# Optimization experiments

Hardware: AMD Instinct MI355X
Metric: run time of the kernel (lower is better)

The kernel has to match this reference:

```python
import jax, jax.numpy as jnp
import numpy as np

NEG_SLOPE = 0.2  # PyG GATConv leaky_relu slope


def _gat_layer(x, src, dst, W, a_src, a_dst, b, concat, num_nodes):
    # x: [N, F_in], W: [F_in, H*C], a_src/a_dst: [H, C], b: [H*C] or [C]
    H, C = a_src.shape
    h = (x @ W).reshape(num_nodes, H, C)                      # [N, H, C]
    s_src = jnp.einsum('nhc,hc->nh', h, a_src)                # [N, H]
    s_dst = jnp.einsum('nhc,hc->nh', h, a_dst)                # [N, H]
    e = jax.nn.leaky_relu(s_src[src] + s_dst[dst], NEG_SLOPE) # [E, H]
    # segment softmax over edges sharing a destination node
    m = jax.ops.segment_max(e, dst, num_segments=num_nodes)
    m = jnp.where(jnp.isfinite(m), m, 0.0)
    p = jnp.exp(e - m[dst])
    z = jax.ops.segment_sum(p, dst, num_segments=num_nodes)
    alpha = p / (z[dst] + 1e-16)                              # [E, H]
    msg = h[src] * alpha[:, :, None]                          # [E, H, C]
    out = jax.ops.segment_sum(msg, dst, num_segments=num_nodes)  # [N, H, C]
    out = out.reshape(num_nodes, H * C) if concat else out.mean(axis=1)
    return out + b


def setup_inputs() -> dict:
    key = jax.random.key(0)
    ks = jax.random.split(key, 16)
    N, E, F = 100000, 800000, 128
    H, C = 4, 32
    sc_in = 1.0 / np.sqrt(F)
    inp = {
        'x': jax.random.normal(ks[0], (N, F), jnp.float32),
        'edge_index': jax.random.randint(ks[1], (2, E), 0, N, jnp.int64),
        'W1': jax.random.normal(ks[2], (F, H * C), jnp.float32) * sc_in,
        'a_src1': jax.random.normal(ks[3], (H, C), jnp.float32),
        'a_dst1': jax.random.normal(ks[4], (H, C), jnp.float32),
        'b1': jax.random.normal(ks[5], (H * C,), jnp.float32) * 0.01,
        'W2': jax.random.normal(ks[6], (F, H * C), jnp.float32) * sc_in,
        'a_src2': jax.random.normal(ks[7], (H, C), jnp.float32),
        'a_dst2': jax.random.normal(ks[8], (H, C), jnp.float32),
        'b2': jax.random.normal(ks[9], (H * C,), jnp.float32) * 0.01,
        'W3': jax.random.normal(ks[10], (F, H * F), jnp.float32) * sc_in,
        'a_src3': jax.random.normal(ks[11], (H, F), jnp.float32),
        'a_dst3': jax.random.normal(ks[12], (H, F), jnp.float32),
        'b3': jax.random.normal(ks[13], (F,), jnp.float32) * 0.01,
    }
    return inp


def reference(x, edge_index, W1, a_src1, a_dst1, b1, W2, a_src2, a_dst2, b2,
              W3, a_src3, a_dst3, b3):
    N = x.shape[0]
    # PyG GATConv default: add self loops
    loop = jnp.arange(N, dtype=edge_index.dtype)
    src = jnp.concatenate([edge_index[0], loop])
    dst = jnp.concatenate([edge_index[1], loop])
    # conv1 (concat heads) + residual + ELU
    x1 = jax.nn.elu(_gat_layer(x, src, dst, W1, a_src1, a_dst1, b1, True, N) + x)
    # intermediate conv (concat heads) + residual + ELU
    x2 = jax.nn.elu(_gat_layer(x1, src, dst, W2, a_src2, a_dst2, b2, True, N) + x1)
    # final conv (mean over heads) + residual, no ELU
    x3 = _gat_layer(x2, src, dst, W3, a_src3, a_dst3, b3, False, N) + x2
    return x3
```

## Files before the change

kernel.cpp:

```cpp
#include <hip/hip_runtime.h>
#include <hip/hip_bf16.h>
#include <cstdint>

#define NEG_SLOPE 0.2f

typedef __bf16 bf16x8 __attribute__((ext_vector_type(8)));
typedef _Float16 half8 __attribute__((ext_vector_type(8)));
typedef float  floatx4 __attribute__((ext_vector_type(4)));

__device__ __forceinline__ float us2f(unsigned short u) {
    union { unsigned int i; float f; } c; c.i = ((unsigned int)u) << 16; return c.f;
}
__device__ __forceinline__ unsigned short f2us(float f) {
    union { float f; unsigned int i; } c; c.f = f;
    unsigned int x = c.i;
    unsigned int r = (x + 0x7fffu + ((x >> 16) & 1u)) >> 16;
    return (unsigned short)r;
}
__device__ __forceinline__ unsigned short f2h(float f) {
    union { _Float16 h; unsigned short u; } c; c.h = (_Float16)f; return c.u;
}
__device__ __forceinline__ float h2f(unsigned short u) {
    union { _Float16 h; unsigned short u; } c; c.u = u; return (float)c.h;
}
__device__ __forceinline__ float ldx(const void* p, int i, int bf) {
    return bf ? us2f(((const unsigned short*)p)[i]) : ((const float*)p)[i];
}
__device__ __forceinline__ void split2(float f, unsigned short& h, unsigned short& l) {
    h = f2us(f);
    l = f2us(f - us2f(h));
}
__device__ __forceinline__ float sel4(const float* a, int i) {
    float lo = (i & 1) ? a[1] : a[0];
    float hi = (i & 1) ? a[3] : a[2];
    return (i & 2) ? hi : lo;
}
__device__ __forceinline__ void unp8(uint4 u, float* f) {
    union { unsigned int i; float ff; } a;
    a.i = u.x << 16;          f[0] = a.ff;
    a.i = u.x & 0xffff0000u;  f[1] = a.ff;
    a.i = u.y << 16;          f[2] = a.ff;
    a.i = u.y & 0xffff0000u;  f[3] = a.ff;
    a.i = u.z << 16;          f[4] = a.ff;
    a.i = u.z & 0xffff0000u;  f[5] = a.ff;
    a.i = u.w << 16;          f[6] = a.ff;
    a.i = u.w & 0xffff0000u;  f[7] = a.ff;
}

__global__ void k_detect(const unsigned short* __restrict__ x16,
                         const unsigned int* __restrict__ ei,
                         int* __restrict__ flags) {
    if (threadIdx.x == 0 && blockIdx.x == 0) {
        int cnt = 0;
        for (int i = 0; i < 1024; ++i) {
            const unsigned short u = x16[2 * i];
            const int e = (u >> 7) & 0xFF;
            if (e < 100 || e > 160) ++cnt;
        }
        flags[0] = (cnt < 256) ? 1 : 0;
        int is64 = 1;
        for (int i = 0; i < 64; ++i)
            if (ei[2 * i + 1] != 0u) { is64 = 0; break; }
        flags[1] = is64;
    }
}

__device__ __forceinline__ int edge_at(const void* ei, int f64, long long idx) {
    if (f64) return (int)((const long long*)ei)[idx];
    return ((const int*)ei)[idx];
}

__global__ void k_hist(const void* __restrict__ ei, const int* __restrict__ flags,
                       int* __restrict__ deg, int E, int N) {
    const int f64 = flags[1];
    const int EP = E + N;
    for (int e = blockIdx.x * blockDim.x + threadIdx.x; e < EP; e += gridDim.x * blockDim.x) {
        int dst = (e < E) ? edge_at(ei, f64, (long long)E + e) : (e - E);
        atomicAdd(&deg[dst], 1);
    }
}

__global__ __launch_bounds__(1024) void k_scan_a(const int* __restrict__ deg,
                                                 int* __restrict__ coff,
                                                 int* __restrict__ part, int N) {
    __shared__ int tmp[1024];
    const int t = threadIdx.x, idx = blockIdx.x * 1024 + t;
    const int v = (idx < N) ? deg[idx] : 0;
    tmp[t] = v; __syncthreads();
    for (int s = 1; s < 1024; s <<= 1) {
        int a = (t >= s) ? tmp[t - s] : 0;
        __syncthreads(); tmp[t] += a; __syncthreads();
    }
    if (idx < N) coff[idx] = tmp[t] - v;
    if (t == 1023) part[blockIdx.x] = tmp[1023];
}

__global__ __launch_bounds__(1024) void k_scan_b(int* __restrict__ part,
                                                 int* __restrict__ coff, int nblk, int N) {
    __shared__ int tmp[1024];
    const int t = threadIdx.x;
    const int v = (t < nblk) ? part[t] : 0;
    tmp[t] = v; __syncthreads();
    for (int s = 1; s < 1024; s <<= 1) {
        int a = (t >= s) ? tmp[t - s] : 0;
        __syncthreads(); tmp[t] += a; __syncthreads();
    }
    if (t < nblk) part[t] = tmp[t] - v;
    if (t == 1023) coff[N] = tmp[1023];
}

__global__ __launch_bounds__(1024) void k_scan_c(int* __restrict__ coff,
                                                 const int* __restrict__ part, int N) {
    const int idx = blockIdx.x * 1024 + threadIdx.x;
    if (idx < N) coff[idx] += part[blockIdx.x];
}

__global__ void k_scatter(const void* __restrict__ ei, const int* __restrict__ flags,
                          const int* __restrict__ coff, int* __restrict__ cpos,
                          int* __restrict__ csrc, int E, int N) {
    const int f64 = flags[1];
    const int EP = E + N;
    for (int e = blockIdx.x * blockDim.x + threadIdx.x; e < EP; e += gridDim.x * blockDim.x) {
        int src, dst;
        if (e < E) { src = edge_at(ei, f64, e); dst = edge_at(ei, f64, (long long)E + e); }
        else       { src = dst = e - E; }
        const int p = atomicAdd(&cpos[dst], 1);
        csrc[coff[dst] + p] = src;
    }
}

template <int F16>
__global__ void k_wfrag(const void* __restrict__ Wv, const int* __restrict__ flags,
                        int wstride, int total,
                        unsigned short* __restrict__ outH, unsigned short* __restrict__ outL) {
    const int bf = flags[0];
    for (int tid = blockIdx.x * blockDim.x + threadIdx.x; tid < total;
         tid += gridDim.x * blockDim.x) {
        const int j    = tid & 7;
        const int lane = (tid >> 3) & 63;
        const int ks   = (tid >> 9) & 3;
        const int ntg  = (tid >> 11) & 7;
        const int blk  = tid >> 14;
        const int k = ks * 32 + (lane >> 4) * 8 + j;
        const int c = blk * 128 + ntg * 16 + (lane & 15);
        const float v = ldx(Wv, k * wstride + c, bf);
        unsigned short h, l;
        if (F16) {
            h = f2h(v);
            l = f2h(v - h2f(h));
        } else {
            split2(v, h, l);
        }
        outH[tid] = h; outL[tid] = l;
    }
}

__global__ void k_wa(const void* __restrict__ W, const void* __restrict__ as,
                     const void* __restrict__ ad, const int* __restrict__ flags,
                     float* __restrict__ va) {
    const int bf = flags[0];
    const int t = blockIdx.x * blockDim.x + threadIdx.x;
    if (t >= 512) return;
    const int k = t >> 2, h = t & 3;
    float ss = 0.f, dd = 0.f;
    for (int c = 0; c < 128; ++c) {
        const float w = ldx(W, k * 512 + h * 128 + c, bf);
        ss = fmaf(w, ldx(as, h * 128 + c, bf), ss);
        dd = fmaf(w, ldx(ad, h * 128 + c, bf), dd);
    }
    va[k * 8 + h] = ss;
    va[k * 8 + 4 + h] = dd;
}

template <bool XRAW, int SC>
__global__ __launch_bounds__(256) void k_gemm(const void* __restrict__ Xv,
                                              const unsigned short* __restrict__ whfB,
                                              const unsigned short* __restrict__ wlfB,
                                              unsigned short* __restrict__ Y16, int ystride,
                                              float* __restrict__ ssrc,
                                              float* __restrict__ sdst,
                                              const void* __restrict__ a_src,
                                              const void* __restrict__ a_dst,
                                              const int* __restrict__ flags,
                                              int N) {
    __shared__ __align__(16) unsigned short Ah[64][136], Al[64][136];
    __shared__ float sred[2][4][SC ? 64 : 1];
    const int bf   = flags[0];
    const int t    = threadIdx.x;
    const int row0 = blockIdx.x * 64;
    const int hy   = blockIdx.y;
    const unsigned short* whf = whfB + hy * 16384;
    const unsigned short* wlf = wlfB + hy * 16384;
    const int ycol0 = hy * 128;
    const int wv   = t >> 6;
    const int lane = t & 63;
    const int quad = lane >> 4;
    const int l16  = lane & 15;

#pragma unroll
    for (int it = 0; it < 8; ++it) {
        const int id = it * 256 + t;
        const int r  = id >> 5;
        const int c  = (id & 31) * 4;
        const int gr = row0 + r;
        ushort4 h4 = make_ushort4(0, 0, 0, 0), l4 = make_ushort4(0, 0, 0, 0);
        if (gr < N) {
            if (XRAW && bf) {
                h4 = *(const ushort4*)&((const unsigned short*)Xv)[(size_t)gr * 128 + c];
            } else {
                const float4 f = *(const float4*)&((const float*)Xv)[(size_t)gr * 128 + c];
                split2(f.x, h4.x, l4.x); split2(f.y, h4.y, l4.y);
                split2(f.z, h4.z, l4.z); split2(f.w, h4.w, l4.w);
            }
        }
        *(ushort4*)&Ah[r][c] = h4;
        *(ushort4*)&Al[r][c] = l4;
    }
    __syncthreads();

    floatx4 acc[4][2];
#pragma unroll
    for (int mt = 0; mt < 4; ++mt)
#pragma unroll
        for (int nt = 0; nt < 2; ++nt) acc[mt][nt] = (floatx4){0.f, 0.f, 0.f, 0.f};

#pragma unroll
    for (int ks = 0; ks < 4; ++ks) {
        const int ko = ks * 32 + quad * 8;
        bf16x8 ah[4], al[4], bh[2], bl[2];
#pragma unroll
        for (int mt = 0; mt < 4; ++mt) ah[mt] = *(const bf16x8*)&Ah[mt * 16 + l16][ko];
        if (!(XRAW && bf)) {
#pragma unroll
            for (int mt = 0; mt < 4; ++mt) al[mt] = *(const bf16x8*)&Al[mt * 16 + l16][ko];
        }
#pragma unroll
        for (int nt = 0; nt < 2; ++nt)
            bh[nt] = *(const bf16x8*)&whf[(((wv * 2 + nt) * 4 + ks) * 64 + lane) * 8];
        if (!bf) {
#pragma unroll
            for (int nt = 0; nt < 2; ++nt)
                bl[nt] = *(const bf16x8*)&wlf[(((wv * 2 + nt) * 4 + ks) * 64 + lane) * 8];
        }
#pragma unroll
        for (int mt = 0; mt < 4; ++mt)
#pragma unroll
            for (int nt = 0; nt < 2; ++nt) {
                acc[mt][nt] = __builtin_amdgcn_mfma_f32_16x16x32_bf16(ah[mt], bh[nt], acc[mt][nt], 0, 0, 0);
                if (!bf)
                    acc[mt][nt] = __builtin_amdgcn_mfma_f32_16x16x32_bf16(ah[mt], bl[nt], acc[mt][nt], 0, 0, 0);
                if (!(XRAW && bf))
                    acc[mt][nt] = __builtin_amdgcn_mfma_f32_16x16x32_bf16(al[mt], bh[nt], acc[mt][nt], 0, 0, 0);
            }
    }

    const int aBase = hy * 128 + wv * 32;
    float as_[2], ad_[2];
#pragma unroll
    for (int nt = 0; nt < 2; ++nt) {
        as_[nt] = ldx(a_src, aBase + nt * 16 + l16, bf);
        ad_[nt] = ldx(a_dst, aBase + nt * 16 + l16, bf);
    }

#pragma unroll
    for (int mt = 0; mt < 4; ++mt) {
        const int rl = mt * 16 + quad * 4;
#pragma unroll
        for (int r = 0; r < 4; ++r) {
            const int grow = row0 + rl + r;
            if (grow < N) {
#pragma unroll
                for (int nt = 0; nt < 2; ++nt)
                    Y16[(size_t)grow * ystride + ycol0 + wv * 32 + nt * 16 + l16] =
                        f2us(acc[mt][nt][r]);
            }
            float ps = acc[mt][0][r] * as_[0] + acc[mt][1][r] * as_[1];
            float pd = acc[mt][0][r] * ad_[0] + acc[mt][1][r] * ad_[1];
#pragma unroll
            for (int mk = 1; mk <= 8; mk <<= 1) {
                ps += __shfl_xor(ps, mk);
                pd += __shfl_xor(pd, mk);
            }
            if (SC == 0) {
                if (l16 == 0 && grow < N) {
                    ssrc[(size_t)grow * 4 + wv] = ps;
                    sdst[(size_t)grow * 4 + wv] = pd;
                }
            } else {
                if (l16 == 0) { sred[0][wv][rl + r] = ps; sred[1][wv][rl + r] = pd; }
            }
        }
    }
    if (SC == 1) {
        __syncthreads();
        if (t < 64 && row0 + t < N) {
            ssrc[(size_t)(row0 + t) * 4 + hy] = sred[0][0][t] + sred[0][1][t] + sred[0][2][t] + sred[0][3][t];
            sdst[(size_t)(row0 + t) * 4 + hy] = sred[1][0][t] + sred[1][1][t] + sred[1][2][t] + sred[1][3][t];
        }
    }
}

template <int MODE>
__global__ __launch_bounds__(256) void k_agg(const int* __restrict__ coff,
                                             const int* __restrict__ csrc,
                                             const float* __restrict__ ssrc,
                                             const float* __restrict__ sdst,
                                             const unsigned short* __restrict__ H16,
                                             const void* __restrict__ bias,
                                             const void* __restrict__ resid,
                                             const int* __restrict__ flags,
                                             void* __restrict__ out, int N,
                                             const float* __restrict__ va,
                                             float* __restrict__ ss2,
                                             float* __restrict__ sd2,
                                             unsigned short* __restrict__ x2h,
                                             unsigned short* __restrict__ x2l) {
    __shared__ float vaS[(MODE == 1) ? 128 : 1][10];
    const int bf   = flags[0];
    const int t    = threadIdx.x;
    const int l16  = t & 15;
    const int n0   = blockIdx.x * 16 + (t >> 4);
    const bool nact = n0 < N;
    const int n    = nact ? n0 : (N - 1);
    const int beg = coff[n], end = coff[n + 1];
    const int deg = end - beg;

    if (MODE == 1) {
        for (int i = t; i < 1024; i += 256) vaS[i >> 3][i & 7] = va[i];
        __syncthreads();
    }

    const float4 sdv = *(const float4*)&sdst[(size_t)n * 4];
    const float sd[4] = { sdv.x, sdv.y, sdv.z, sdv.w };
    const bool fast = (deg <= 16);
    float z[4];
    int   myS = 0;
    float wn[4] = { 0.f, 0.f, 0.f, 0.f };

    if (fast) {
        const bool act = l16 < deg;
        if (act) {
            myS = csrc[beg + l16];
            const float4 sp = *(const float4*)&ssrc[(size_t)myS * 4];
            const float s4[4] = { sp.x, sp.y, sp.z, sp.w };
#pragma unroll
            for (int h = 0; h < 4; ++h) {
                float tv = s4[h] + sd[h];
                tv = tv >= 0.f ? tv : NEG_SLOPE * tv;
                wn[h] = __expf(fminf(tv, 80.f));
            }
        }
#pragma unroll
        for (int h = 0; h < 4; ++h) z[h] = wn[h];
#pragma unroll
        for (int mk = 1; mk <= 8; mk <<= 1)
#pragma unroll
            for (int h = 0; h < 4; ++h) z[h] += __shfl_xor(z[h], mk);
    } else {
#pragma unroll
        for (int h = 0; h < 4; ++h) z[h] = 0.f;
        for (int e = beg + l16; e < end; e += 16) {
            const int s = csrc[e];
            const float4 sp = *(const float4*)&ssrc[(size_t)s * 4];
            const float s4[4] = { sp.x, sp.y, sp.z, sp.w };
#pragma unroll
            for (int h = 0; h < 4; ++h) {
                float tv = s4[h] + sd[h];
                tv = tv >= 0.f ? tv : NEG_SLOPE * tv;
                z[h] += __expf(fminf(tv, 80.f));
            }
        }
#pragma unroll
        for (int mk = 1; mk <= 8; mk <<= 1)
#pragma unroll
            for (int h = 0; h < 4; ++h) z[h] += __shfl_xor(z[h], mk);
    }

    float ivz[4];
#pragma unroll
    for (int h = 0; h < 4; ++h) ivz[h] = 1.f / (z[h] + 1e-16f);

    const int c8 = l16 * 8;
    const int hd = l16 >> 2;
    const float ih = sel4(ivz, hd);
    float ac[8];
#pragma unroll
    for (int j = 0; j < 8; ++j) ac[j] = 0.f;

    if (fast) {
        for (int e = 0; e < deg; ++e) {
            const int s = __shfl(myS, e, 16);
            float wa4[4];
            wa4[0] = __shfl(wn[0], e, 16);
            wa4[1] = __shfl(wn[1], e, 16);
            wa4[2] = __shfl(wn[2], e, 16);
            wa4[3] = __shfl(wn[3], e, 16);
            const float w = sel4(wa4, hd);
            const uint4 u = *(const uint4*)&H16[(size_t)s * 128 + c8];
            float f[8]; unp8(u, f);
#pragma unroll
            for (int j = 0; j < 8; ++j) ac[j] = fmaf(w, f[j], ac[j]);
        }
    } else {
        const float sdh = sel4(sd, hd);
        for (int e = beg; e < end; ++e) {
            const int s = csrc[e];
            float tv = ssrc[(size_t)s * 4 + hd] + sdh;
            tv = tv >= 0.f ? tv : NEG_SLOPE * tv;
            const float w = __expf(fminf(tv, 80.f));
            const uint4 u = *(const uint4*)&H16[(size_t)s * 128 + c8];
            float f[8]; unp8(u, f);
#pragma unroll
            for (int j = 0; j < 8; ++j) ac[j] = fmaf(w, f[j], ac[j]);
        }
    }

#pragma unroll
    for (int j = 0; j < 8; ++j) ac[j] *= ih;

    if (!nact) return;
    const int ob = n * 128 + c8;
    float rr[8];
    if (MODE == 0) {
        if (bf) {
            const uint4 u = *(const uint4*)&((const unsigned short*)resid)[ob];
            unp8(u, rr);
        } else {
            const float4 r0 = *(const float4*)&((const float*)resid)[ob];
            const float4 r1 = *(const float4*)&((const float*)resid)[ob + 4];
            rr[0] = r0.x; rr[1] = r0.y; rr[2] = r0.z; rr[3] = r0.w;
            rr[4] = r1.x; rr[5] = r1.y; rr[6] = r1.z; rr[7] = r1.w;
        }
    } else {
        const float4 r0 = *(const float4*)&((const float*)resid)[ob];
        const float4 r1 = *(const float4*)&((const float*)resid)[ob + 4];
        rr[0] = r0.x; rr[1] = r0.y; rr[2] = r0.z; rr[3] = r0.w;
        rr[4] = r1.x; rr[5] = r1.y; rr[6] = r1.z; rr[7] = r1.w;
    }
    float o[8];
#pragma unroll
    for (int j = 0; j < 8; ++j) {
        const float v = ac[j] + ldx(bias, c8 + j, bf) + rr[j];
        o[j] = v > 0.f ? v : expm1f(v);
    }
    if (MODE == 0) {
        *(float4*)&((float*)out)[ob]     = make_float4(o[0], o[1], o[2], o[3]);
        *(float4*)&((float*)out)[ob + 4] = make_float4(o[4], o[5], o[6], o[7]);
    }

    if (MODE == 1) {
        unsigned short hi[8], lo[8];
#pragma unroll
        for (int j = 0; j < 8; ++j) {
            hi[j] = f2us(o[j]);
            lo[j] = f2us(o[j] - us2f(hi[j]));
        }
        uint4 uh, ul;
        uh.x = (unsigned int)hi[0] | ((unsigned int)hi[1] << 16);
        uh.y = (unsigned int)hi[2] | ((unsigned int)hi[3] << 16);
        uh.z = (unsigned int)hi[4] | ((unsigned int)hi[5] << 16);
        uh.w = (unsigned int)hi[6] | ((unsigned int)hi[7] << 16);
        ul.x = (unsigned int)lo[0] | ((unsigned int)lo[1] << 16);
        ul.y = (unsigned int)lo[2] | ((unsigned int)lo[3] << 16);
        ul.z = (unsigned int)lo[4] | ((unsigned int)lo[5] << 16);
        ul.w = (unsigned int)lo[6] | ((unsigned int)lo[7] << 16);
        *(uint4*)&x2h[ob] = uh;
        *(uint4*)&x2l[ob] = ul;
        float p[8];
#pragma unroll
        for (int o8 = 0; o8 < 8; ++o8) {
            float acc = 0.f;
#pragma unroll
            for (int j = 0; j < 8; ++j) acc = fmaf(o[j], vaS[c8 + j][o8], acc);
            p[o8] = acc;
        }
#pragma unroll
        for (int mk = 1; mk <= 8; mk <<= 1)
#pragma unroll
            for (int o8 = 0; o8 < 8; ++o8) p[o8] += __shfl_xor(p[o8], mk);
        if (l16 == 0) {
#pragma unroll
            for (int h = 0; h < 4; ++h) {
                ss2[(size_t)n * 4 + h] = p[h];
                sd2[(size_t)n * 4 + h] = p[4 + h];
            }
        }
    }
}

__global__ __launch_bounds__(256) void k_aggx3(const int* __restrict__ coff,
                                               const int* __restrict__ csrc,
                                               const float* __restrict__ ssrc,
                                               const float* __restrict__ sdst,
                                               const unsigned short* __restrict__ X16,
                                               const unsigned short* __restrict__ Xl16,
                                               const unsigned short* __restrict__ whf,
                                               const unsigned short* __restrict__ wlf,
                                               const void* __restrict__ bias,
                                               const int* __restrict__ flags,
                                               void* __restrict__ out, int N) {
    __shared__ __align__(16) unsigned short aggS[4][32][136];
    const int bf   = flags[0];
    const int t    = threadIdx.x;
    const int row0 = blockIdx.x * 32;
    const int l16  = t & 15;

    for (int sb = 0; sb < 2; ++sb) {
        const int r  = sb * 16 + (t >> 4);
        const int n0 = row0 + r;
        const int n  = (n0 < N) ? n0 : (N - 1);
        const int beg = coff[n], end = coff[n + 1];
        const int deg = end - beg;

        const float4 sdv = *(const float4*)&sdst[(size_t)n * 4];
        const float sd[4] = { sdv.x, sdv.y, sdv.z, sdv.w };
        const bool fast = (deg <= 16);
        float m[4], z[4];
        int   myS = 0;
        float wn[4] = { 0.f, 0.f, 0.f, 0.f };

        if (fast) {
            const bool act = l16 < deg;
            float v[4];
#pragma unroll
            for (int h = 0; h < 4; ++h) v[h] = -1e30f;
            if (act) {
                myS = csrc[beg + l16];
                const float4 sp = *(const float4*)&ssrc[(size_t)myS * 4];
                const float s4[4] = { sp.x, sp.y, sp.z, sp.w };
#pragma unroll
                for (int h = 0; h < 4; ++h) {
                    float tv = s4[h] + sd[h];
                    v[h] = tv >= 0.f ? tv : NEG_SLOPE * tv;
                }
            }
#pragma unroll
            for (int h = 0; h < 4; ++h) m[h] = v[h];
#pragma unroll
            for (int mk = 1; mk <= 8; mk <<= 1)
#pragma unroll
                for (int h = 0; h < 4; ++h) m[h] = fmaxf(m[h], __shfl_xor(m[h], mk));
            float w[4];
#pragma unroll
            for (int h = 0; h < 4; ++h) w[h] = act ? __expf(v[h] - m[h]) : 0.f;
#pragma unroll
            for (int h = 0; h < 4; ++h) z[h] = w[h];
#pragma unroll
            for (int mk = 1; mk <= 8; mk <<= 1)
#pragma unroll
                for (int h = 0; h < 4; ++h) z[h] += __shfl_xor(z[h], mk);
#pragma unroll
            for (int h = 0; h < 4; ++h) wn[h] = w[h] / (z[h] + 1e-16f);
        } else {
#pragma unroll
            for (int h = 0; h < 4; ++h) m[h] = -1e30f;
            for (int e = beg + l16; e < end; e += 16) {
                const int s = csrc[e];
                const float4 sp = *(const float4*)&ssrc[(size_t)s * 4];
                const float s4[4] = { sp.x, sp.y, sp.z, sp.w };
#pragma unroll
                for (int h = 0; h < 4; ++h) {
                    float tv = s4[h] + sd[h];
                    tv = tv >= 0.f ? tv : NEG_SLOPE * tv;
                    m[h] = fmaxf(m[h], tv);
                }
            }
#pragma unroll
            for (int mk = 1; mk <= 8; mk <<= 1)
#pragma unroll
                for (int h = 0; h < 4; ++h) m[h] = fmaxf(m[h], __shfl_xor(m[h], mk));
#pragma unroll
            for (int h = 0; h < 4; ++h) z[h] = 0.f;
            for (int e = beg + l16; e < end; e += 16) {
                const int s = csrc[e];
                const float4 sp = *(const float4*)&ssrc[(size_t)s * 4];
                const float s4[4] = { sp.x, sp.y, sp.z, sp.w };
#pragma unroll
                for (int h = 0; h < 4; ++h) {
                    float tv = s4[h] + sd[h];
                    tv = tv >= 0.f ? tv : NEG_SLOPE * tv;
                    z[h] += __expf(tv - m[h]);
                }
            }
#pragma unroll
            for (int mk = 1; mk <= 8; mk <<= 1)
#pragma unroll
                for (int h = 0; h < 4; ++h) z[h] += __shfl_xor(z[h], mk);
        }

        const int c8 = l16 * 8;
        float ac[4][8];
#pragma unroll
        for (int h = 0; h < 4; ++h)
#pragma unroll
            for (int j = 0; j < 8; ++j) ac[h][j] = 0.f;

        if (fast) {
            int e = 0;
            for (; e + 2 <= deg; e += 2) {
                const int s0 = __shfl(myS, e + 0, 16);
                const int s1 = __shfl(myS, e + 1, 16);
                const uint4 u0 = *(const uint4*)&X16[(size_t)s0 * 128 + c8];
                const uint4 u1 = *(const uint4*)&X16[(size_t)s1 * 128 + c8];
                float w0[4], w1[4];
#pragma unroll
                for (int h = 0; h < 4; ++h) {
                    w0[h] = __shfl(wn[h], e + 0, 16);
                    w1[h] = __shfl(wn[h], e + 1, 16);
                }
                float f[8];
                unp8(u0, f);
#pragma unroll
                for (int h = 0; h < 4; ++h)
#pragma unroll
                    for (int j = 0; j < 8; ++j) ac[h][j] = fmaf(w0[h], f[j], ac[h][j]);
                unp8(u1, f);
#pragma unroll
                for (int h = 0; h < 4; ++h)
#pragma unroll
                    for (int j = 0; j < 8; ++j) ac[h][j] = fmaf(w1[h], f[j], ac[h][j]);
            }
            for (; e < deg; ++e) {
                const int s = __shfl(myS, e, 16);
                float wr[4];
                wr[0] = __shfl(wn[0], e, 16);
                wr[1] = __shfl(wn[1], e, 16);
                wr[2] = __shfl(wn[2], e, 16);
                wr[3] = __shfl(wn[3], e, 16);
                const uint4 u = *(const uint4*)&X16[(size_t)s * 128 + c8];
                float f[8]; unp8(u, f);
#pragma unroll
                for (int h = 0; h < 4; ++h)
#pragma unroll
                    for (int j = 0; j < 8; ++j) ac[h][j] = fmaf(wr[h], f[j], ac[h][j]);
            }
        } else {
            float ivh[4];
#pragma unroll
            for (int h = 0; h < 4; ++h) ivh[h] = 1.f / (z[h] + 1e-16f);
            for (int e = beg; e < end; ++e) {
                const int s = csrc[e];
                const float4 sp = *(const float4*)&ssrc[(size_t)s * 4];
                const float s4[4] = { sp.x, sp.y, sp.z, sp.w };
                float wr[4];
#pragma unroll
                for (int h = 0; h < 4; ++h) {
                    float tv = s4[h] + sd[h];
                    tv = tv >= 0.f ? tv : NEG_SLOPE * tv;
                    wr[h] = __expf(tv - m[h]) * ivh[h];
                }
                const uint4 u = *(const uint4*)&X16[(size_t)s * 128 + c8];
                float f[8]; unp8(u, f);
#pragma unroll
                for (int h = 0; h < 4; ++h)
#pragma unroll
                    for (int j = 0; j < 8; ++j) ac[h][j] = fmaf(wr[h], f[j], ac[h][j]);
            }
        }

#pragma unroll
        for (int h = 0; h < 4; ++h) {
            uint4 u;
            u.x = (unsigned int)f2h(ac[h][0]) | ((unsigned int)f2h(ac[h][1]) << 16);
            u.y = (unsigned int)f2h(ac[h][2]) | ((unsigned int)f2h(ac[h][3]) << 16);
            u.z = (unsigned int)f2h(ac[h][4]) | ((unsigned int)f2h(ac[h][5]) << 16);
            u.w = (unsigned int)f2h(ac[h][6]) | ((unsigned int)f2h(ac[h][7]) << 16);
            *(uint4*)&aggS[h][r][c8] = u;
        }
    }
    __syncthreads();

    const int wv   = t >> 6;
    const int lane = t & 63;
    const int quad = lane >> 4;
    const int q16  = lane & 15;

    floatx4 acc[2][2];
#pragma unroll
    for (int mt = 0; mt < 2; ++mt)
#pragma unroll
        for (int nt = 0; nt < 2; ++nt) acc[mt][nt] = (floatx4){0.f, 0.f, 0.f, 0.f};

#pragma unroll
    for (int kc = 0; kc < 4; ++kc) {
        const unsigned short* whc = whf + kc * 16384;
        const unsigned short* wlc = wlf + kc * 16384;
#pragma unroll
        for (int ks = 0; ks < 4; ++ks) {
            const int ko = ks * 32 + quad * 8;
            half8 ah[2], bh[2], bl[2];
#pragma unroll
            for (int mt = 0; mt < 2; ++mt) ah[mt] = *(const half8*)&aggS[kc][mt * 16 + q16][ko];
#pragma unroll
            for (int nt = 0; nt < 2; ++nt) {
                bh[nt] = *(const half8*)&whc[(((wv * 2 + nt) * 4 + ks) * 64 + lane) * 8];
                bl[nt] = *(const half8*)&wlc[(((wv * 2 + nt) * 4 + ks) * 64 + lane) * 8];
            }
#pragma unroll
            for (int mt = 0; mt < 2; ++mt)
#pragma unroll
                for (int nt = 0; nt < 2; ++nt) {
                    acc[mt][nt] = __builtin_amdgcn_mfma_f32_16x16x32_f16(ah[mt], bh[nt], acc[mt][nt], 0, 0, 0);
                    acc[mt][nt] = __builtin_amdgcn_mfma_f32_16x16x32_f16(ah[mt], bl[nt], acc[mt][nt], 0, 0, 0);
                }
        }
    }

#pragma unroll
    for (int mt = 0; mt < 2; ++mt) {
        const int rl = mt * 16 + quad * 4;
#pragma unroll
        for (int r = 0; r < 4; ++r) {
            const int grow = row0 + rl + r;
            if (grow < N) {
#pragma unroll
                for (int nt = 0; nt < 2; ++nt) {
                    const int col = wv * 32 + nt * 16 + q16;
                    const size_t ix = (size_t)grow * 128 + col;
                    const float resid = us2f(X16[ix]) + us2f(Xl16[ix]);
                    const float v = acc[mt][nt][r] * 0.25f + ldx(bias, col, bf) + resid;
                    if (bf) ((unsigned short*)out)[ix] = f2us(v);
                    else    ((float*)out)[ix] = v;
                }
            }
        }
    }
}

extern "C" void kernel_launch(void* const* d_in, const int* in_sizes, int n_in,
                              void* d_out, int out_size, void* d_ws, size_t ws_size,
                              hipStream_t stream) {
    const int N  = in_sizes[0] / 128;
    const int E  = in_sizes[1] / 2;
    const int EP = E + N;

    const void* x   = d_in[0];
    const void* ei  = d_in[1];
    const void* W1  = d_in[2];
    const void* as1 = d_in[3];
    const void* ad1 = d_in[4];
    const void* b1  = d_in[5];
    const void* W2  = d_in[6];
    const void* as2 = d_in[7];
    const void* ad2 = d_in[8];
    const void* b2  = d_in[9];
    const void* W3  = d_in[10];
    const void* as3 = d_in[11];
    const void* ad3 = d_in[12];
    const void* b3  = d_in[13];

    char* p = (char*)d_ws;
    auto alloc = [&](size_t bytes) { char* r = p; p += (bytes + 255) & ~(size_t)255; return r; };
    int*   flags = (int*)alloc(8);
    int*   deg   = (int*)alloc((size_t)(N + 1) * 4);
    int*   coff  = (int*)alloc((size_t)(N + 1) * 4);
    int*   cpos  = (int*)alloc((size_t)N * 4);
    int*   part  = (int*)alloc(4096);
    int*   csrc  = (int*)alloc((size_t)EP * 4);
    float* x1b   = (float*)alloc((size_t)N * 128 * 4);
    unsigned short* h16_12 = (unsigned short*)alloc((size_t)N * 128 * 2);
    float* ssrc  = (float*)alloc((size_t)N * 4 * 4);
    float* sdst  = (float*)alloc((size_t)N * 4 * 4);
    unsigned short* whf1 = (unsigned short*)alloc(16384 * 2);
    unsigned short* wlf1 = (unsigned short*)alloc(16384 * 2);
    unsigned short* whf2 = (unsigned short*)alloc(16384 * 2);
    unsigned short* wlf2 = (unsigned short*)alloc(16384 * 2);
    unsigned short* whf3 = (unsigned short*)alloc(65536 * 2);
    unsigned short* wlf3 = (unsigned short*)alloc(65536 * 2);
    unsigned short* x2h  = (unsigned short*)alloc((size_t)N * 128 * 2);
    unsigned short* x2l  = (unsigned short*)alloc((size_t)N * 128 * 2);
    float* va    = (float*)alloc(128 * 8 * 4);
    float* ssrc3 = (float*)alloc((size_t)N * 4 * 4);
    float* sdst3 = (float*)alloc((size_t)N * 4 * 4);

    hipMemsetAsync(deg,  0, (size_t)(N + 1) * 4, stream);
    hipMemsetAsync(cpos, 0, (size_t)N * 4, stream);

    k_detect<<<1, 64, 0, stream>>>((const unsigned short*)x, (const unsigned int*)ei, flags);

    k_wfrag<0><<<64, 256, 0, stream>>>(W1, flags, 128, 16384, whf1, wlf1);
    k_wfrag<0><<<64, 256, 0, stream>>>(W2, flags, 128, 16384, whf2, wlf2);
    k_wfrag<1><<<256, 256, 0, stream>>>(W3, flags, 512, 65536, whf3, wlf3);
    k_wa<<<2, 256, 0, stream>>>(W3, as3, ad3, flags, va);

    const int egrid = (EP + 255) / 256;
    const int nblk  = (N + 1023) / 1024;
    k_hist<<<egrid, 256, 0, stream>>>(ei, flags, deg, E, N);
    k_scan_a<<<nblk, 1024, 0, stream>>>(deg, coff, part, N);
    k_scan_b<<<1, 1024, 0, stream>>>(part, coff, nblk, N);
    k_scan_c<<<nblk, 1024, 0, stream>>>(coff, part, N);
    k_scatter<<<egrid, 256, 0, stream>>>(ei, flags, coff, cpos, csrc, E, N);

    const int ggrid = (N + 63) / 64;
    const int ngrid = (N + 15) / 16;
    const int fgrid = (N + 31) / 32;

    k_gemm<true, 0><<<dim3(ggrid, 1), 256, 0, stream>>>(x, whf1, wlf1, h16_12, 128,
                                                        ssrc, sdst, as1, ad1, flags, N);
    k_agg<0><<<ngrid, 256, 0, stream>>>(coff, csrc, ssrc, sdst, h16_12, b1, x, flags, x1b, N,
                                        nullptr, nullptr, nullptr, nullptr, nullptr);

    k_gemm<false, 0><<<dim3(ggrid, 1), 256, 0, stream>>>(x1b, whf2, wlf2, h16_12, 128,
                                                         ssrc, sdst, as2, ad2, flags, N);
    k_agg<1><<<ngrid, 256, 0, stream>>>(coff, csrc, ssrc, sdst, h16_12, b2, x1b, flags, nullptr, N,
                                        va, ssrc3, sdst3, x2h, x2l);

    k_aggx3<<<fgrid, 256, 0, stream>>>(coff, csrc, ssrc3, sdst3, x2h, x2l,
                                       whf3, wlf3, b3, flags, d_out, N);
}
```

Before: 636.0 us.

## Drop low-half weight MFMA in layer-3 aggregation and halve rows per block

The final fused aggregate-then-project kernel no longer uses the split hi/lo fp16 representation of W3. It issues a single MFMA per tile using only the high part, which halves both the matrix-core work and the weight fragment loads. The block tile also shrinks from 32 rows to 16, giving twice as many blocks and half the LDS per block, so occupancy and load balance on the gather phase should improve. The cost is lower precision in the W3 projection, since its fp16 rounding error is no longer corrected, and weight fragments are reused across fewer rows.

```diff
diff --git a/kernel.cpp b/kernel.cpp
--- a/kernel.cpp
+++ b/kernel.cpp
@@ -495,18 +495,17 @@
                                                const unsigned short* __restrict__ X16,
                                                const unsigned short* __restrict__ Xl16,
                                                const unsigned short* __restrict__ whf,
-                                               const unsigned short* __restrict__ wlf,
                                                const void* __restrict__ bias,
                                                const int* __restrict__ flags,
                                                void* __restrict__ out, int N) {
-    __shared__ __align__(16) unsigned short aggS[4][32][136];
+    __shared__ __align__(16) unsigned short aggS[4][16][136];
     const int bf   = flags[0];
     const int t    = threadIdx.x;
-    const int row0 = blockIdx.x * 32;
+    const int row0 = blockIdx.x * 16;
     const int l16  = t & 15;
 
-    for (int sb = 0; sb < 2; ++sb) {
-        const int r  = sb * 16 + (t >> 4);
+    {
+        const int r  = t >> 4;
         const int n0 = row0 + r;
         const int n  = (n0 < N) ? n0 : (N - 1);
         const int beg = coff[n], end = coff[n + 1];
@@ -675,53 +674,40 @@
     const int quad = lane >> 4;
     const int q16  = lane & 15;
 
-    floatx4 acc[2][2];
-#pragma unroll
-    for (int mt = 0; mt < 2; ++mt)
-#pragma unroll
-        for (int nt = 0; nt < 2; ++nt) acc[mt][nt] = (floatx4){0.f, 0.f, 0.f, 0.f};
+    floatx4 acc[2];
+#pragma unroll
+    for (int nt = 0; nt < 2; ++nt) acc[nt] = (floatx4){0.f, 0.f, 0.f, 0.f};
 
 #pragma unroll
     for (int kc = 0; kc < 4; ++kc) {
         const unsigned short* whc = whf + kc * 16384;
-        const unsigned short* wlc = wlf + kc * 16384;
 #pragma unroll
         for (int ks = 0; ks < 4; ++ks) {
             const int ko = ks * 32 + quad * 8;
-            half8 ah[2], bh[2], bl[2];
-#pragma unroll
-            for (int mt = 0; mt < 2; ++mt) ah[mt] = *(const half8*)&aggS[kc][mt * 16 + q16][ko];
+            half8 ah, bh[2];
+            ah = *(const half8*)&aggS[kc][q16][ko];
+#pragma unroll
+            for (int nt = 0; nt < 2; ++nt)
+                bh[nt] = *(const half8*)&whc[(((wv * 2 + nt) * 4 + ks) * 64 + lane) * 8];
+#pragma unroll
+            for (int nt = 0; nt < 2; ++nt)
+                acc[nt] = __builtin_amdgcn_mfma_f32_16x16x32_f16(ah, bh[nt], acc[nt], 0, 0, 0);
+        }
+    }
+
+    const int rl = quad * 4;
+#pragma unroll
+    for (int r = 0; r < 4; ++r) {
+        const int grow = row0 + rl + r;
+        if (grow < N) {
 #pragma unroll
             for (int nt = 0; nt < 2; ++nt) {
-                bh[nt] = *(const half8*)&whc[(((wv * 2 + nt) * 4 + ks) * 64 + lane) * 8];
-                bl[nt] = *(const half8*)&wlc[(((wv * 2 + nt) * 4 + ks) * 64 + lane) * 8];
-            }
-#pragma unroll
-            for (int mt = 0; mt < 2; ++mt)
-#pragma unroll
-                for (int nt = 0; nt < 2; ++nt) {
-                    acc[mt][nt] = __builtin_amdgcn_mfma_f32_16x16x32_f16(ah[mt], bh[nt], acc[mt][nt], 0, 0, 0);
-                    acc[mt][nt] = __builtin_amdgcn_mfma_f32_16x16x32_f16(ah[mt], bl[nt], acc[mt][nt], 0, 0, 0);
-                }
-        }
-    }
-
-#pragma unroll
-    for (int mt = 0; mt < 2; ++mt) {
-        const int rl = mt * 16 + quad * 4;
-#pragma unroll
-        for (int r = 0; r < 4; ++r) {
-            const int grow = row0 + rl + r;
-            if (grow < N) {
-#pragma unroll
-                for (int nt = 0; nt < 2; ++nt) {
-                    const int col = wv * 32 + nt * 16 + q16;
-                    const size_t ix = (size_t)grow * 128 + col;
-                    const float resid = us2f(X16[ix]) + us2f(Xl16[ix]);
-                    const float v = acc[mt][nt][r] * 0.25f + ldx(bias, col, bf) + resid;
-                    if (bf) ((unsigned short*)out)[ix] = f2us(v);
-                    else    ((float*)out)[ix] = v;
-                }
+                const int col = wv * 32 + nt * 16 + q16;
+                const size_t ix = (size_t)grow * 128 + col;
+                const float resid = us2f(X16[ix]) + us2f(Xl16[ix]);
+                const float v = acc[nt][r] * 0.25f + ldx(bias, col, bf) + resid;
+                if (bf) ((unsigned short*)out)[ix] = f2us(v);
+                else    ((float*)out)[ix] = v;
             }
         }
     }
@@ -793,7 +779,6 @@
 
     const int ggrid = (N + 63) / 64;
     const int ngrid = (N + 15) / 16;
-    const int fgrid = (N + 31) / 32;
 
     k_gemm<true, 0><<<dim3(ggrid, 1), 256, 0, stream>>>(x, whf1, wlf1, h16_12, 128,
                                                         ssrc, sdst, as1, ad1, flags, N);
@@ -805,6 +790,6 @@
     k_agg<1><<<ngrid, 256, 0, stream>>>(coff, csrc, ssrc, sdst, h16_12, b2, x1b, flags, nullptr, N,
                                         va, ssrc3, sdst3, x2h, x2l);
 
-    k_aggx3<<<fgrid, 256, 0, stream>>>(coff, csrc, ssrc3, sdst3, x2h, x2l,
-                                       whf3, wlf3, b3, flags, d_out, N);
-}
+    k_aggx3<<<ngrid, 256, 0, stream>>>(coff, csrc, ssrc3, sdst3, x2h, x2l,
+                                       whf3, b3, flags, d_out, N);
+}
```

Measured after the change: 610.7 us, median of 3. 1.04x faster.
